# Kernel optimization log

Hardware: AMD Instinct MI355X
Metric: run time of the kernel (lower is better)

## Reference

```python
import jax, jax.numpy as jnp
import numpy as np

N_NODES = 50000
N_EDGES = 800000
D_IN = 128
HIDDEN = [128, 128]
D_OUT = 64


def setup_inputs() -> dict:
    key = jax.random.key(0)
    ks = jax.random.split(key, 12)
    x = jax.random.normal(ks[0], (N_NODES, D_IN), dtype=jnp.float32)
    edge_index = jax.random.randint(ks[1], (2, N_EDGES), 0, N_NODES, dtype=jnp.int64)
    # SAGEConv params: lin_l acts on aggregated neighbors (has bias), lin_r on root
    def lin(k, fan_in, fan_out):
        s = 1.0 / np.sqrt(fan_in)
        return jax.random.uniform(k, (fan_in, fan_out), jnp.float32, -s, s)
    dims = [D_IN] + HIDDEN
    inp = {"x": x, "edge_index": edge_index}
    for i in range(len(HIDDEN)):
        inp[f"Wl{i}"] = lin(ks[2 + 3 * i], dims[i], dims[i + 1])
        inp[f"Wr{i}"] = lin(ks[3 + 3 * i], dims[i], dims[i + 1])
        inp[f"b{i}"] = jnp.zeros((dims[i + 1],), jnp.float32)
    inp["Wfc"] = lin(ks[10], HIDDEN[-1], D_OUT)
    inp["bfc"] = jnp.zeros((D_OUT,), jnp.float32)
    return inp


def _sage_conv(x, src, dst, n, Wl, Wr, b, deg_inv):
    # mean-aggregate source features into destination nodes
    agg = jax.ops.segment_sum(x[src], dst, num_segments=n) * deg_inv[:, None]
    return agg @ Wl + x @ Wr + b


def reference(x, edge_index, Wl0, Wr0, b0, Wl1, Wr1, b1, Wfc, bfc):
    src, dst = edge_index[0], edge_index[1]
    n = x.shape[0]
    deg = jax.ops.segment_sum(jnp.ones((src.shape[0],), x.dtype), dst, num_segments=n)
    deg_inv = 1.0 / jnp.maximum(deg, 1.0)
    h = jax.nn.relu(_sage_conv(x, src, dst, n, Wl0, Wr0, b0, deg_inv))
    # dropout p=0 / eval mode -> identity
    h = jax.nn.relu(_sage_conv(h, src, dst, n, Wl1, Wr1, b1, deg_inv))
    return h @ Wfc + bfc
```

## Files before the change

### kernel.cpp

```cpp
#include <hip/hip_runtime.h>
#include <hip/hip_bf16.h>

#define NN 50000
#define NE 800000
#define D 128
#define DOUT 64
#define PAD 64
#define BSH 8
#define NBUCK 196
#define CAP 4608
#define CHUNK 4096

typedef __attribute__((ext_vector_type(8))) short short8;
typedef __attribute__((ext_vector_type(4))) float float4v;


__device__ inline unsigned short f2bf(float f) {
    union { float f; unsigned int i; } c; c.f = f;
    unsigned int u = c.i;
    return (unsigned short)((u + 0x7fffu + ((u >> 16) & 1u)) >> 16);
}
__device__ inline float bflo(unsigned int u) {
    union { unsigned int i; float f; } c; c.i = u << 16; return c.f;
}
__device__ inline float bfhi(unsigned int u) {
    union { unsigned int i; float f; } c; c.i = u & 0xffff0000u; return c.f;
}


__global__ void cast_f32_bf16(const float* __restrict__ in, unsigned short* __restrict__ outb, int n8) {
    int i = blockIdx.x * 256 + threadIdx.x;
    if (i >= n8) return;
    const float4* p = (const float4*)in + (size_t)i * 2;
    float4 a = p[0], b = p[1];
    unsigned int w0 = f2bf(a.x) | ((unsigned int)f2bf(a.y) << 16);
    unsigned int w1 = f2bf(a.z) | ((unsigned int)f2bf(a.w) << 16);
    unsigned int w2 = f2bf(b.x) | ((unsigned int)f2bf(b.y) << 16);
    unsigned int w3 = f2bf(b.z) | ((unsigned int)f2bf(b.w) << 16);
    *(uint4*)(outb + (size_t)i * 8) = make_uint4(w0, w1, w2, w3);
}


struct PackArgs {
    const float* W[5];
    unsigned short* P[5];
};

__global__ void pack_all(PackArgs args) {
    int idx = blockIdx.x * 256 + threadIdx.x;
    if (idx >= 4 * 2048 + 1024) return;
    const float* W;
    unsigned short* P;
    int COLS, local;
    if (idx < 4 * 2048) {
        int wsel = idx >> 11;
        W = args.W[wsel]; P = args.P[wsel]; COLS = 128; local = idx & 2047;
    } else {
        W = args.W[4]; P = args.P[4]; COLS = 64; local = idx - 4 * 2048;
    }
    int CT = COLS >> 4;
    int lane = local & 63;
    int fi = local >> 6;
    int ct = fi % CT;
    int kstep = fi / CT;
    int krow = kstep * 32 + (lane >> 4) * 8;
    int col = ct * 16 + (lane & 15);
    unsigned short v[8];
#pragma unroll
    for (int j = 0; j < 8; ++j) v[j] = f2bf(W[(size_t)(krow + j) * COLS + col]);
    unsigned int w0 = v[0] | ((unsigned int)v[1] << 16);
    unsigned int w1 = v[2] | ((unsigned int)v[3] << 16);
    unsigned int w2 = v[4] | ((unsigned int)v[5] << 16);
    unsigned int w3 = v[6] | ((unsigned int)v[7] << 16);
    *(uint4*)(P + (size_t)local * 8) = make_uint4(w0, w1, w2, w3);
}


__global__ void bin_edges(const int* __restrict__ src, const int* __restrict__ dst,
                          int* __restrict__ gcur, unsigned int* __restrict__ binned, int e) {
    __shared__ int cnt[NBUCK];
    __shared__ int sh[256];
    __shared__ int baseg[NBUCK];
    __shared__ int lcur[NBUCK];
    __shared__ unsigned int buf[CHUNK];
    int tid = threadIdx.x;
    int base = blockIdx.x * CHUNK;
    for (int b = tid; b < NBUCK; b += 256) cnt[b] = 0;
    __syncthreads();
    unsigned int rec[16];
#pragma unroll
    for (int i = 0; i < 16; ++i) {
        int ei = base + i * 256 + tid;
        rec[i] = 0xffffffffu;
        if (ei < e) {
            unsigned int d = (unsigned int)dst[ei];
            unsigned int s = (unsigned int)src[ei];
            rec[i] = (d << 16) | s;
            atomicAdd(&cnt[d >> BSH], 1);
        }
    }
    __syncthreads();
    int v = (tid < NBUCK) ? cnt[tid] : 0;
    sh[tid] = v;
    __syncthreads();
    for (int off = 1; off < 256; off <<= 1) {
        int t = (tid >= off) ? sh[tid - off] : 0;
        __syncthreads();
        sh[tid] += t;
        __syncthreads();
    }
    if (tid < NBUCK) {
        baseg[tid] = atomicAdd(&gcur[tid], cnt[tid]);
        lcur[tid] = sh[tid] - cnt[tid];
    }
    __syncthreads();
    int total = sh[255];
#pragma unroll
    for (int i = 0; i < 16; ++i) {
        if (rec[i] != 0xffffffffu) {
            int b = rec[i] >> 24;
            int pos = atomicAdd(&lcur[b], 1);
            buf[pos] = rec[i];
        }
    }
    __syncthreads();
    for (int j = tid; j < total; j += 256) {
        unsigned int r = buf[j];
        int b = r >> 24;
        int gidx = baseg[b] + (j - (sh[b] - cnt[b]));
        if (gidx < CAP) binned[(size_t)b * CAP + gidx] = r;
    }
}


__global__ void scatter_bucket(const unsigned int* __restrict__ binned, const int* __restrict__ gcur,
                               unsigned short* __restrict__ eidx_pad, int* __restrict__ cursor) {
    __shared__ int cur[256];
    int b = blockIdx.x;
    int tid = threadIdx.x;
    cur[tid] = 0;
    __syncthreads();
    int count = gcur[b];
    if (count > CAP) count = CAP;
    const unsigned int* seg = binned + (size_t)b * CAP;
    for (int j = tid; j < count; j += 256) {
        unsigned int r = seg[j];
        int dl = (r >> 16) & 255;
        int slot = atomicAdd(&cur[dl], 1);
        if (slot < PAD)
            eidx_pad[((size_t)((b << BSH) + dl)) * PAD + slot] = (unsigned short)(r & 0xffffu);
    }
    __syncthreads();
    int node = (b << BSH) + tid;
    if (node < NN) cursor[node] = (cur[tid] < PAD) ? cur[tid] : PAD;
}


__global__ void aggregate_bf(const unsigned short* __restrict__ feat, unsigned short* __restrict__ out,
                             const int* __restrict__ cursor, const unsigned short* __restrict__ eidx_pad,
                             int n) {
    int node = blockIdx.x * 4 + (threadIdx.x >> 6);
    if (node >= n) return;
    int lane = threadIdx.x & 63;
    int q = lane >> 4;
    int c = lane & 15;
    int deg = cursor[node];
    float di = 1.0f / (float)(deg > 1 ? deg : 1);
    const unsigned short* row = eidx_pad + (size_t)node * PAD;
    float acc[8] = {0.f, 0.f, 0.f, 0.f, 0.f, 0.f, 0.f, 0.f};
    int p = q;
    for (; p + 4 < deg; p += 8) {
        int s0 = row[p];
        int s1 = row[p + 4];
        uint4 v0 = *(const uint4*)(feat + (size_t)s0 * D + c * 8);
        uint4 v1 = *(const uint4*)(feat + (size_t)s1 * D + c * 8);
        acc[0] += bflo(v0.x) + bflo(v1.x); acc[1] += bfhi(v0.x) + bfhi(v1.x);
        acc[2] += bflo(v0.y) + bflo(v1.y); acc[3] += bfhi(v0.y) + bfhi(v1.y);
        acc[4] += bflo(v0.z) + bflo(v1.z); acc[5] += bfhi(v0.z) + bfhi(v1.z);
        acc[6] += bflo(v0.w) + bflo(v1.w); acc[7] += bfhi(v0.w) + bfhi(v1.w);
    }
    if (p < deg) {
        int s = row[p];
        uint4 v = *(const uint4*)(feat + (size_t)s * D + c * 8);
        acc[0] += bflo(v.x); acc[1] += bfhi(v.x);
        acc[2] += bflo(v.y); acc[3] += bfhi(v.y);
        acc[4] += bflo(v.z); acc[5] += bfhi(v.z);
        acc[6] += bflo(v.w); acc[7] += bfhi(v.w);
    }
#pragma unroll
    for (int j = 0; j < 8; ++j) {
        acc[j] += __shfl_down(acc[j], 32);
        acc[j] += __shfl_down(acc[j], 16);
    }
    if (q == 0) {
        unsigned int w0 = f2bf(acc[0] * di) | ((unsigned int)f2bf(acc[1] * di) << 16);
        unsigned int w1 = f2bf(acc[2] * di) | ((unsigned int)f2bf(acc[3] * di) << 16);
        unsigned int w2 = f2bf(acc[4] * di) | ((unsigned int)f2bf(acc[5] * di) << 16);
        unsigned int w3 = f2bf(acc[6] * di) | ((unsigned int)f2bf(acc[7] * di) << 16);
        *(uint4*)(out + (size_t)node * D + c * 8) = make_uint4(w0, w1, w2, w3);
    }
}


template <bool FUSEFC>
__global__ void mfma_gemm(const unsigned short* __restrict__ A, const unsigned short* __restrict__ X,
                          const unsigned short* __restrict__ Pl, const unsigned short* __restrict__ Pr,
                          const float* __restrict__ bias,
                          const unsigned short* __restrict__ Pfc, const float* __restrict__ bfc,
                          unsigned short* __restrict__ outb, float* __restrict__ outf, int n) {
    __shared__ __align__(16) unsigned short As[64][136];
    __shared__ __align__(16) unsigned short Xs[64][136];

    int tid = threadIdx.x;
    int row0 = blockIdx.x * 64;

    for (int v = tid; v < 1024; v += 256) {
        int r = v >> 4;
        int c8 = (v & 15) * 8;
        int gr = row0 + r;
        uint4 av = make_uint4(0, 0, 0, 0), xv = av;
        if (gr < n) {
            av = *(const uint4*)(A + (size_t)gr * D + c8);
            xv = *(const uint4*)(X + (size_t)gr * D + c8);
        }
        *(uint4*)&As[r][c8] = av;
        *(uint4*)&Xs[r][c8] = xv;
    }
    __syncthreads();

    int wave = tid >> 6;
    int lane = tid & 63;
    int m16 = lane & 15;
    int quad = lane >> 4;
    int rt0 = (wave & 1) * 32;
    int ctb = (wave >> 1) * 4;

    float4v acc[2][4];
#pragma unroll
    for (int t = 0; t < 2; ++t)
#pragma unroll
        for (int c = 0; c < 4; ++c) acc[t][c] = (float4v){0.f, 0.f, 0.f, 0.f};

#pragma unroll
    for (int ks = 0; ks < 4; ++ks) {
        short8 af[2];
#pragma unroll
        for (int t = 0; t < 2; ++t)
            af[t] = *(const short8*)&As[rt0 + t * 16 + m16][ks * 32 + quad * 8];
#pragma unroll
        for (int c = 0; c < 4; ++c) {
            short8 bf = *(const short8*)(Pl + ((size_t)((ks * 8 + ctb + c) * 64 + lane)) * 8);
#pragma unroll
            for (int t = 0; t < 2; ++t)
                acc[t][c] = __builtin_amdgcn_mfma_f32_16x16x32_bf16(af[t], bf, acc[t][c], 0, 0, 0);
        }
    }
#pragma unroll
    for (int ks = 0; ks < 4; ++ks) {
        short8 xf[2];
#pragma unroll
        for (int t = 0; t < 2; ++t)
            xf[t] = *(const short8*)&Xs[rt0 + t * 16 + m16][ks * 32 + quad * 8];
#pragma unroll
        for (int c = 0; c < 4; ++c) {
            short8 bf = *(const short8*)(Pr + ((size_t)((ks * 8 + ctb + c) * 64 + lane)) * 8);
#pragma unroll
            for (int t = 0; t < 2; ++t)
                acc[t][c] = __builtin_amdgcn_mfma_f32_16x16x32_bf16(xf[t], bf, acc[t][c], 0, 0, 0);
        }
    }

    if (!FUSEFC) {
#pragma unroll
        for (int t = 0; t < 2; ++t) {
#pragma unroll
            for (int c = 0; c < 4; ++c) {
                int col = (ctb + c) * 16 + m16;
                float bv = bias[col];
#pragma unroll
                for (int i = 0; i < 4; ++i) {
                    int row = row0 + rt0 + t * 16 + quad * 4 + i;
                    if (row < n)
                        outb[(size_t)row * D + col] = f2bf(fmaxf(acc[t][c][i] + bv, 0.f));
                }
            }
        }
    } else {
        __syncthreads();
#pragma unroll
        for (int t = 0; t < 2; ++t) {
#pragma unroll
            for (int c = 0; c < 4; ++c) {
                int col = (ctb + c) * 16 + m16;
                float bv = bias[col];
#pragma unroll
                for (int i = 0; i < 4; ++i) {
                    int row = rt0 + t * 16 + quad * 4 + i;
                    As[row][col] = f2bf(fmaxf(acc[t][c][i] + bv, 0.f));
                }
            }
        }
        __syncthreads();

        int ctbF = (wave >> 1) * 2;
        float4v acc2[2][2];
#pragma unroll
        for (int t = 0; t < 2; ++t)
#pragma unroll
            for (int c = 0; c < 2; ++c) acc2[t][c] = (float4v){0.f, 0.f, 0.f, 0.f};
#pragma unroll
        for (int ks = 0; ks < 4; ++ks) {
            short8 hf[2];
#pragma unroll
            for (int t = 0; t < 2; ++t)
                hf[t] = *(const short8*)&As[rt0 + t * 16 + m16][ks * 32 + quad * 8];
#pragma unroll
            for (int c = 0; c < 2; ++c) {
                short8 bf = *(const short8*)(Pfc + ((size_t)((ks * 4 + ctbF + c) * 64 + lane)) * 8);
#pragma unroll
                for (int t = 0; t < 2; ++t)
                    acc2[t][c] = __builtin_amdgcn_mfma_f32_16x16x32_bf16(hf[t], bf, acc2[t][c], 0, 0, 0);
            }
        }
#pragma unroll
        for (int t = 0; t < 2; ++t) {
#pragma unroll
            for (int c = 0; c < 2; ++c) {
                int col = (ctbF + c) * 16 + m16;
                float bv = bfc[col];
#pragma unroll
                for (int i = 0; i < 4; ++i) {
                    int row = row0 + rt0 + t * 16 + quad * 4 + i;
                    if (row < n)
                        outf[(size_t)row * DOUT + col] = acc2[t][c][i] + bv;
                }
            }
        }
    }
}


extern "C" void kernel_launch(void* const* d_in, const int* in_sizes, int n_in,
                              void* d_out, int out_size, void* d_ws, size_t ws_size,
                              hipStream_t stream) {
    const float* x   = (const float*)d_in[0];
    const int*   ei  = (const int*)d_in[1];
    const float* Wl0 = (const float*)d_in[2];
    const float* Wr0 = (const float*)d_in[3];
    const float* b0  = (const float*)d_in[4];
    const float* Wl1 = (const float*)d_in[5];
    const float* Wr1 = (const float*)d_in[6];
    const float* b1  = (const float*)d_in[7];
    const float* Wfc = (const float*)d_in[8];
    const float* bfc = (const float*)d_in[9];
    float* out = (float*)d_out;

    const int* src = ei;
    const int* dst = ei + NE;

    char* p = (char*)d_ws;
    auto carve = [&](size_t bytes) {
        char* q = p;
        p += (bytes + 255) & ~(size_t)255;
        return q;
    };
    int*            cursor   = (int*)carve(NN * sizeof(int));
    int*            gcur     = (int*)carve(NBUCK * sizeof(int));
    unsigned int*   binned   = (unsigned int*)carve((size_t)NBUCK * CAP * 4);
    unsigned short* eidx_pad = (unsigned short*)carve((size_t)NN * PAD * 2);
    unsigned short* xb   = (unsigned short*)carve((size_t)NN * D * 2);
    unsigned short* aggb = (unsigned short*)carve((size_t)NN * D * 2);
    unsigned short* h0b  = (unsigned short*)carve((size_t)NN * D * 2);
    unsigned short* Wl0p = (unsigned short*)carve(D * D * 2);
    unsigned short* Wr0p = (unsigned short*)carve(D * D * 2);
    unsigned short* Wl1p = (unsigned short*)carve(D * D * 2);
    unsigned short* Wr1p = (unsigned short*)carve(D * D * 2);
    unsigned short* Wfcp = (unsigned short*)carve(D * DOUT * 2);

    hipMemsetAsync(gcur, 0, NBUCK * sizeof(int), stream);

    const int N8 = NN * D / 8;
    cast_f32_bf16<<<(N8 + 255) / 256, 256, 0, stream>>>(x, xb, N8);

    PackArgs pa;
    pa.W[0] = Wl0; pa.W[1] = Wr0; pa.W[2] = Wl1; pa.W[3] = Wr1; pa.W[4] = Wfc;
    pa.P[0] = Wl0p; pa.P[1] = Wr0p; pa.P[2] = Wl1p; pa.P[3] = Wr1p; pa.P[4] = Wfcp;
    pack_all<<<(4 * 2048 + 1024 + 255) / 256, 256, 0, stream>>>(pa);

    const int BINB = (NE + CHUNK - 1) / CHUNK;
    bin_edges<<<BINB, 256, 0, stream>>>(src, dst, gcur, binned, NE);
    scatter_bucket<<<NBUCK, 256, 0, stream>>>(binned, gcur, eidx_pad, cursor);

    const int AGB = (NN + 3) / 4;
    const int GB  = (NN + 63) / 64;

    aggregate_bf<<<AGB, 256, 0, stream>>>(xb, aggb, cursor, eidx_pad, NN);
    mfma_gemm<false><<<GB, 256, 0, stream>>>(aggb, xb, Wl0p, Wr0p, b0, nullptr, nullptr, h0b, nullptr, NN);
    aggregate_bf<<<AGB, 256, 0, stream>>>(h0b, aggb, cursor, eidx_pad, NN);
    mfma_gemm<true><<<GB, 256, 0, stream>>>(aggb, h0b, Wl1p, Wr1p, b1, Wfcp, bfc, nullptr, out, NN);
}
```

Before: 205.0 us.

## Fuse neighbor mean aggregation into the SAGE layer GEMM kernel

Removes the separate aggregation kernel and gathers and averages neighbor features directly into shared memory inside the MFMA GEMM block, so the intermediate aggregated buffer is never written to or read back from global memory. Each 64-row block now gathers its rows with 16 threads per node, four nodes per thread group, unrolled by four edges. This cuts two launches and the aggregate round trip. In exchange, the gather runs at the lower occupancy of the GEMM kernel (large shared memory footprint), which may reduce latency hiding for the random gathers.

```diff
diff --git a/kernel.cpp b/kernel.cpp
--- a/kernel.cpp
+++ b/kernel.cpp
@@ -156,58 +156,13 @@
 }
 
 
-__global__ void aggregate_bf(const unsigned short* __restrict__ feat, unsigned short* __restrict__ out,
-                             const int* __restrict__ cursor, const unsigned short* __restrict__ eidx_pad,
-                             int n) {
-    int node = blockIdx.x * 4 + (threadIdx.x >> 6);
-    if (node >= n) return;
-    int lane = threadIdx.x & 63;
-    int q = lane >> 4;
-    int c = lane & 15;
-    int deg = cursor[node];
-    float di = 1.0f / (float)(deg > 1 ? deg : 1);
-    const unsigned short* row = eidx_pad + (size_t)node * PAD;
-    float acc[8] = {0.f, 0.f, 0.f, 0.f, 0.f, 0.f, 0.f, 0.f};
-    int p = q;
-    for (; p + 4 < deg; p += 8) {
-        int s0 = row[p];
-        int s1 = row[p + 4];
-        uint4 v0 = *(const uint4*)(feat + (size_t)s0 * D + c * 8);
-        uint4 v1 = *(const uint4*)(feat + (size_t)s1 * D + c * 8);
-        acc[0] += bflo(v0.x) + bflo(v1.x); acc[1] += bfhi(v0.x) + bfhi(v1.x);
-        acc[2] += bflo(v0.y) + bflo(v1.y); acc[3] += bfhi(v0.y) + bfhi(v1.y);
-        acc[4] += bflo(v0.z) + bflo(v1.z); acc[5] += bfhi(v0.z) + bfhi(v1.z);
-        acc[6] += bflo(v0.w) + bflo(v1.w); acc[7] += bfhi(v0.w) + bfhi(v1.w);
-    }
-    if (p < deg) {
-        int s = row[p];
-        uint4 v = *(const uint4*)(feat + (size_t)s * D + c * 8);
-        acc[0] += bflo(v.x); acc[1] += bfhi(v.x);
-        acc[2] += bflo(v.y); acc[3] += bfhi(v.y);
-        acc[4] += bflo(v.z); acc[5] += bfhi(v.z);
-        acc[6] += bflo(v.w); acc[7] += bfhi(v.w);
-    }
-#pragma unroll
-    for (int j = 0; j < 8; ++j) {
-        acc[j] += __shfl_down(acc[j], 32);
-        acc[j] += __shfl_down(acc[j], 16);
-    }
-    if (q == 0) {
-        unsigned int w0 = f2bf(acc[0] * di) | ((unsigned int)f2bf(acc[1] * di) << 16);
-        unsigned int w1 = f2bf(acc[2] * di) | ((unsigned int)f2bf(acc[3] * di) << 16);
-        unsigned int w2 = f2bf(acc[4] * di) | ((unsigned int)f2bf(acc[5] * di) << 16);
-        unsigned int w3 = f2bf(acc[6] * di) | ((unsigned int)f2bf(acc[7] * di) << 16);
-        *(uint4*)(out + (size_t)node * D + c * 8) = make_uint4(w0, w1, w2, w3);
-    }
-}
-
-
 template <bool FUSEFC>
-__global__ void mfma_gemm(const unsigned short* __restrict__ A, const unsigned short* __restrict__ X,
-                          const unsigned short* __restrict__ Pl, const unsigned short* __restrict__ Pr,
-                          const float* __restrict__ bias,
-                          const unsigned short* __restrict__ Pfc, const float* __restrict__ bfc,
-                          unsigned short* __restrict__ outb, float* __restrict__ outf, int n) {
+__global__ void fused_layer(const unsigned short* __restrict__ feat,
+                            const int* __restrict__ cursor, const unsigned short* __restrict__ eidx_pad,
+                            const unsigned short* __restrict__ Pl, const unsigned short* __restrict__ Pr,
+                            const float* __restrict__ bias,
+                            const unsigned short* __restrict__ Pfc, const float* __restrict__ bfc,
+                            unsigned short* __restrict__ outb, float* __restrict__ outf, int n) {
     __shared__ __align__(16) unsigned short As[64][136];
     __shared__ __align__(16) unsigned short Xs[64][136];
 
@@ -218,13 +173,55 @@
         int r = v >> 4;
         int c8 = (v & 15) * 8;
         int gr = row0 + r;
-        uint4 av = make_uint4(0, 0, 0, 0), xv = av;
-        if (gr < n) {
-            av = *(const uint4*)(A + (size_t)gr * D + c8);
-            xv = *(const uint4*)(X + (size_t)gr * D + c8);
-        }
-        *(uint4*)&As[r][c8] = av;
+        uint4 xv = make_uint4(0, 0, 0, 0);
+        if (gr < n) xv = *(const uint4*)(feat + (size_t)gr * D + c8);
         *(uint4*)&Xs[r][c8] = xv;
+    }
+
+    {
+        int g = tid >> 4;
+        int l = tid & 15;
+#pragma unroll
+        for (int nn = 0; nn < 4; ++nn) {
+            int r = g * 4 + nn;
+            int node = row0 + r;
+            float acc[8] = {0.f, 0.f, 0.f, 0.f, 0.f, 0.f, 0.f, 0.f};
+            float di = 1.f;
+            if (node < n) {
+                int deg = cursor[node];
+                di = 1.0f / (float)(deg > 1 ? deg : 1);
+                const unsigned short* rowp = eidx_pad + (size_t)node * PAD;
+                int p = 0;
+                for (; p + 3 < deg; p += 4) {
+                    int s0 = rowp[p], s1 = rowp[p + 1], s2 = rowp[p + 2], s3 = rowp[p + 3];
+                    uint4 v0 = *(const uint4*)(feat + (size_t)s0 * D + l * 8);
+                    uint4 v1 = *(const uint4*)(feat + (size_t)s1 * D + l * 8);
+                    uint4 v2 = *(const uint4*)(feat + (size_t)s2 * D + l * 8);
+                    uint4 v3 = *(const uint4*)(feat + (size_t)s3 * D + l * 8);
+                    acc[0] += (bflo(v0.x) + bflo(v1.x)) + (bflo(v2.x) + bflo(v3.x));
+                    acc[1] += (bfhi(v0.x) + bfhi(v1.x)) + (bfhi(v2.x) + bfhi(v3.x));
+                    acc[2] += (bflo(v0.y) + bflo(v1.y)) + (bflo(v2.y) + bflo(v3.y));
+                    acc[3] += (bfhi(v0.y) + bfhi(v1.y)) + (bfhi(v2.y) + bfhi(v3.y));
+                    acc[4] += (bflo(v0.z) + bflo(v1.z)) + (bflo(v2.z) + bflo(v3.z));
+                    acc[5] += (bfhi(v0.z) + bfhi(v1.z)) + (bfhi(v2.z) + bfhi(v3.z));
+                    acc[6] += (bflo(v0.w) + bflo(v1.w)) + (bflo(v2.w) + bflo(v3.w));
+                    acc[7] += (bfhi(v0.w) + bfhi(v1.w)) + (bfhi(v2.w) + bfhi(v3.w));
+                }
+                for (; p < deg; ++p) {
+                    int s = rowp[p];
+                    uint4 v0 = *(const uint4*)(feat + (size_t)s * D + l * 8);
+                    acc[0] += bflo(v0.x); acc[1] += bfhi(v0.x);
+                    acc[2] += bflo(v0.y); acc[3] += bfhi(v0.y);
+                    acc[4] += bflo(v0.z); acc[5] += bfhi(v0.z);
+                    acc[6] += bflo(v0.w); acc[7] += bfhi(v0.w);
+                }
+            }
+            unsigned int w0 = f2bf(acc[0] * di) | ((unsigned int)f2bf(acc[1] * di) << 16);
+            unsigned int w1 = f2bf(acc[2] * di) | ((unsigned int)f2bf(acc[3] * di) << 16);
+            unsigned int w2 = f2bf(acc[4] * di) | ((unsigned int)f2bf(acc[5] * di) << 16);
+            unsigned int w3 = f2bf(acc[6] * di) | ((unsigned int)f2bf(acc[7] * di) << 16);
+            *(uint4*)&As[r][l * 8] = make_uint4(w0, w1, w2, w3);
+        }
     }
     __syncthreads();
 
@@ -369,7 +366,6 @@
     unsigned int*   binned   = (unsigned int*)carve((size_t)NBUCK * CAP * 4);
     unsigned short* eidx_pad = (unsigned short*)carve((size_t)NN * PAD * 2);
     unsigned short* xb   = (unsigned short*)carve((size_t)NN * D * 2);
-    unsigned short* aggb = (unsigned short*)carve((size_t)NN * D * 2);
     unsigned short* h0b  = (unsigned short*)carve((size_t)NN * D * 2);
     unsigned short* Wl0p = (unsigned short*)carve(D * D * 2);
     unsigned short* Wr0p = (unsigned short*)carve(D * D * 2);
@@ -391,11 +387,10 @@
     bin_edges<<<BINB, 256, 0, stream>>>(src, dst, gcur, binned, NE);
     scatter_bucket<<<NBUCK, 256, 0, stream>>>(binned, gcur, eidx_pad, cursor);
 
-    const int AGB = (NN + 3) / 4;
-    const int GB  = (NN + 63) / 64;
-
-    aggregate_bf<<<AGB, 256, 0, stream>>>(xb, aggb, cursor, eidx_pad, NN);
-    mfma_gemm<false><<<GB, 256, 0, stream>>>(aggb, xb, Wl0p, Wr0p, b0, nullptr, nullptr, h0b, nullptr, NN);
-    aggregate_bf<<<AGB, 256, 0, stream>>>(h0b, aggb, cursor, eidx_pad, NN);
-    mfma_gemm<true><<<GB, 256, 0, stream>>>(aggb, h0b, Wl1p, Wr1p, b1, Wfcp, bfc, nullptr, out, NN);
-}
+    const int GB = (NN + 63) / 64;
+
+    fused_layer<false><<<GB, 256, 0, stream>>>(xb, cursor, eidx_pad, Wl0p, Wr0p, b0,
+                                               nullptr, nullptr, h0b, nullptr, NN);
+    fused_layer<true><<<GB, 256, 0, stream>>>(h0b, cursor, eidx_pad, Wl1p, Wr1p, b1,
+                                              Wfcp, bfc, nullptr, out, NN);
+}
```

After: 199.1 us. 1.03x faster.
